# Kernel tuning notes

Measured on AMD Instinct MI355X. Metric: run time of the kernel, lower is better.

## Reference

```python
import jax, jax.numpy as jnp
import numpy as np

NH = 4  # attention heads

def rmsnorm(x, w, eps=1e-5):
    return x * jax.lax.rsqrt(jnp.mean(x * x, axis=-1, keepdims=True) + eps) * w

def gin(x, src, dst, W, b):
    # GINConv(eps=0): Linear(x + sum_{j->i} x_j)
    agg = jax.ops.segment_sum(x[src], dst, num_segments=x.shape[0])
    return (x + agg) @ W + b

def attn_pool(xb, vt, qkv_w, qkv_b, ao_w, ao_b):
    # xb: [B, Nmax, H] padded nodes (zeros participate, matching the torch code
    # which passes no key_padding_mask); vt: [T, H] virtual tokens.
    B, Nmax, H = xb.shape
    T = vt.shape[0]
    hd = H // NH
    q = (vt @ qkv_w[:, :H] + qkv_b[:H]).reshape(T, NH, hd)
    k = (xb @ qkv_w[:, H:2 * H] + qkv_b[H:2 * H]).reshape(B, Nmax, NH, hd)
    v = (xb @ qkv_w[:, 2 * H:] + qkv_b[2 * H:]).reshape(B, Nmax, NH, hd)
    scores = jnp.einsum('thd,bkhd->bhtk', q, k) / jnp.sqrt(jnp.asarray(hd, xb.dtype))
    attn = jax.nn.softmax(scores, axis=-1)
    o = jnp.einsum('bhtk,bkhd->bthd', attn, v).reshape(B, T, H)
    return o @ ao_w + ao_b

def mamba(tokens, in_w, conv_w, conv_b, x_w, dt_w, dt_b, A_log, D, out_w, norm_w, normf_w):
    # HF MambaModel with num_hidden_layers=1 (slow path), inputs_embeds path.
    B, T, H = tokens.shape
    I, K = conv_w.shape
    S = A_log.shape[1]
    R = dt_w.shape[0]
    res = tokens
    h = rmsnorm(tokens, norm_w)
    proj = h @ in_w                      # [B,T,2I]
    u, gate = jnp.split(proj, 2, axis=-1)
    up = jnp.pad(u, ((0, 0), (K - 1, 0), (0, 0)))  # causal depthwise conv1d
    conv = sum(conv_w[:, k] * up[:, k:k + T, :] for k in range(K)) + conv_b
    u = jax.nn.silu(conv)                # [B,T,I]
    ssm = u @ x_w                        # [B,T,R+2S]
    dtr, Bm, Cm = jnp.split(ssm, [R, R + S], axis=-1)
    dt = jax.nn.softplus(dtr @ dt_w + dt_b)  # [B,T,I]
    A = -jnp.exp(A_log)                  # [I,S]

    def step(hstate, inp):
        dt_t, B_t, C_t, u_t = inp        # [B,I],[B,S],[B,S],[B,I]
        dA = jnp.exp(dt_t[:, :, None] * A)
        dBu = dt_t[:, :, None] * B_t[:, None, :] * u_t[:, :, None]
        hstate = dA * hstate + dBu
        y = jnp.sum(hstate * C_t[:, None, :], axis=-1)
        return hstate, y

    h0 = jnp.zeros((B, I, S), tokens.dtype)
    xs = (dt.transpose(1, 0, 2), Bm.transpose(1, 0, 2), Cm.transpose(1, 0, 2), u.transpose(1, 0, 2))
    _, ys = jax.lax.scan(step, h0, xs)
    y = ys.transpose(1, 0, 2) + u * D
    y = y * jax.nn.silu(gate)
    out = y @ out_w                      # [B,T,H]
    return rmsnorm(res + out, normf_w)

def _forward(x, edge_index, batch, num_graphs, nodes_per_graph,
             w_in, b_in, gin_w, gin_b, vt, qkv_w, qkv_b, ao_w, ao_b,
             m_in_w, m_conv_w, m_conv_b, m_x_w, m_dt_w, m_dt_b,
             m_A_log, m_D, m_out_w, m_norm_w, m_normf_w, w_out, b_out):
    src, dst = edge_index[0], edge_index[1]
    N = x.shape[0]
    starts = jnp.searchsorted(batch, jnp.arange(num_graphs, dtype=batch.dtype))
    pos = jnp.arange(N, dtype=batch.dtype) - starts[batch]
    x = gin(x, src, dst, w_in, b_in)
    H = x.shape[-1]
    for l in range(gin_w.shape[0]):
        g = gin(x, src, dst, gin_w[l], gin_b[l])
        xb = jnp.zeros((num_graphs, nodes_per_graph, H), x.dtype).at[batch, pos].set(x)
        tokens = attn_pool(xb, vt[l], qkv_w[l], qkv_b[l], ao_w[l], ao_b[l])
        gf = mamba(tokens, m_in_w, m_conv_w, m_conv_b, m_x_w, m_dt_w, m_dt_b,
                   m_A_log, m_D, m_out_w, m_norm_w, m_normf_w)
        x = g + gf.mean(axis=1)[batch]
    x = gin(x, src, dst, w_out, b_out)
    return jax.ops.segment_sum(x, batch, num_segments=num_graphs)

def setup_inputs() -> dict:
    key = jax.random.key(0)
    ks = jax.random.split(key, 24)
    N, E, B, NPG = 131072, 2097152, 128, 1024
    IN = H = OUT = 128
    T, L = 8, 2
    I, S, R, K = 256, 16, 8, 4  # mamba: intermediate, state, dt_rank, conv kernel
    w = lambda k, s: (jax.random.normal(k, s, jnp.float32) * 0.02)
    x = jax.random.normal(ks[0], (N, IN), jnp.float32)
    edge_index = jax.random.randint(ks[1], (2, E), 0, N, jnp.int32)
    batch = (jnp.arange(N) // NPG).astype(jnp.int32)
    return dict(
        x=x, edge_index=edge_index, batch=batch, num_graphs=B, nodes_per_graph=NPG,
        w_in=w(ks[2], (IN, H)), b_in=jnp.zeros((H,), jnp.float32),
        gin_w=w(ks[3], (L, H, H)), gin_b=jnp.zeros((L, H), jnp.float32),
        vt=jax.random.normal(ks[4], (L, T, H), jnp.float32),
        qkv_w=w(ks[5], (L, H, 3 * H)), qkv_b=jnp.zeros((L, 3 * H), jnp.float32),
        ao_w=w(ks[6], (L, H, H)), ao_b=jnp.zeros((L, H), jnp.float32),
        m_in_w=w(ks[7], (H, 2 * I)),
        m_conv_w=w(ks[8], (I, K)), m_conv_b=jnp.zeros((I,), jnp.float32),
        m_x_w=w(ks[9], (I, R + 2 * S)),
        m_dt_w=w(ks[10], (R, I)), m_dt_b=jnp.full((I,), 0.1, jnp.float32),
        m_A_log=jnp.log(jnp.tile(jnp.arange(1, S + 1, dtype=jnp.float32), (I, 1))),
        m_D=jnp.ones((I,), jnp.float32),
        m_out_w=w(ks[11], (I, H)),
        m_norm_w=jnp.ones((H,), jnp.float32), m_normf_w=jnp.ones((H,), jnp.float32),
        w_out=w(ks[12], (H, OUT)), b_out=jnp.zeros((OUT,), jnp.float32),
    )

def reference(x, edge_index, batch, num_graphs, nodes_per_graph,
              w_in, b_in, gin_w, gin_b, vt, qkv_w, qkv_b, ao_w, ao_b,
              m_in_w, m_conv_w, m_conv_b, m_x_w, m_dt_w, m_dt_b,
              m_A_log, m_D, m_out_w, m_norm_w, m_normf_w, w_out, b_out):
    return _forward(x, edge_index, batch, num_graphs, nodes_per_graph,
                    w_in, b_in, gin_w, gin_b, vt, qkv_w, qkv_b, ao_w, ao_b,
                    m_in_w, m_conv_w, m_conv_b, m_x_w, m_dt_w, m_dt_b,
                    m_A_log, m_D, m_out_w, m_norm_w, m_normf_w, w_out, b_out)
```

## Files before the change

### kernel.cpp

```cpp
#include <hip/hip_runtime.h>

#define HDIM 128
#define TTOK 8
#define NPG 1024
#define NBUCK 512
#define BSHIFT 8
#define BCAP 5120
#define EPB 4096
#define PARTSZ 4160

typedef unsigned short ushort;
typedef unsigned int uint;
typedef __attribute__((ext_vector_type(8))) short short8;
typedef __attribute__((ext_vector_type(4))) float f32x4;

__device__ __forceinline__ ushort f2bf(float f) {
    unsigned int x = __float_as_uint(f);
    return (ushort)((x + 0x7FFFu + ((x >> 16) & 1u)) >> 16);
}
__device__ __forceinline__ float blo(uint u) { return __uint_as_float(u << 16); }
__device__ __forceinline__ float bhi(uint u) { return __uint_as_float(u & 0xFFFF0000u); }
__device__ __forceinline__ uint pk(float a, float b) {
    return (uint)f2bf(a) | ((uint)f2bf(b) << 16);
}

__global__ __launch_bounds__(256) void bin_kernel(const int* __restrict__ src,
    const int* __restrict__ dst, int mode, int* __restrict__ bcursor,
    uint* __restrict__ pairbuf, int E)
{
    __shared__ int lcnt[NBUCK];
    __shared__ int lbase[NBUCK];
    int tid = threadIdx.x;
    int e0 = blockIdx.x * EPB;
    for (int i = tid; i < NBUCK; i += 256) lcnt[i] = 0;
    __syncthreads();
    uint pkd[16];
    int bk[16], rk[16];
    #pragma unroll
    for (int i = 0; i < 16; ++i) {
        int e = e0 + i * 256 + tid;
        int s = (e < E) ? src[e] : 0;
        int d = (e < E) ? dst[e] : 0;
        int key = mode ? s : d;
        uint pay = mode ? (uint)(d >> 10) : (uint)s;
        if (e >= E) key = -1;
        int b = key >> BSHIFT;
        bk[i] = b;
        pkd[i] = ((uint)(key & 255) << 17) | pay;
        rk[i] = (key >= 0) ? atomicAdd(&lcnt[b], 1) : 0;
    }
    __syncthreads();
    for (int i = tid; i < NBUCK; i += 256) {
        int c = lcnt[i];
        lbase[i] = c ? atomicAdd(&bcursor[i], c) : 0;
    }
    __syncthreads();
    #pragma unroll
    for (int i = 0; i < 16; ++i) {
        if (bk[i] >= 0) {
            int slot = lbase[bk[i]] + rk[i];
            if (slot < BCAP) pairbuf[(size_t)bk[i] * BCAP + slot] = pkd[i];
        }
    }
}

__global__ __launch_bounds__(256) void bucket_sort_kernel(const uint* __restrict__ pairbuf,
    const int* __restrict__ bcount,
    int* __restrict__ ssrc, int* __restrict__ starts, int* __restrict__ countn, int N)
{
    __shared__ int sc[NBUCK];
    __shared__ int lcount[256];
    __shared__ int lcur[256];
    __shared__ int lss[BCAP];
    int b = blockIdx.x;
    int tid = threadIdx.x;
    sc[tid] = min(bcount[tid], BCAP);
    sc[tid + 256] = min(bcount[tid + 256], BCAP);
    lcount[tid] = 0;
    __syncthreads();
    for (int off = 1; off < NBUCK; off <<= 1) {
        int a0 = (tid >= off) ? sc[tid - off] : 0;
        int a1 = (tid + 256 >= off) ? sc[tid + 256 - off] : 0;
        __syncthreads();
        sc[tid] += a0; sc[tid + 256] += a1;
        __syncthreads();
    }
    int nb = min(bcount[b], BCAP);
    int base = sc[b] - nb;
    const uint* pp = pairbuf + (size_t)b * BCAP;
    for (int i = tid; i < nb; i += 256)
        atomicAdd(&lcount[(pp[i] >> 17) & 255], 1);
    __syncthreads();
    int v = lcount[tid];
    lcur[tid] = v;
    __syncthreads();
    for (int off = 1; off < 256; off <<= 1) {
        int t = (tid >= off) ? lcur[tid - off] : 0;
        __syncthreads();
        lcur[tid] += t;
        __syncthreads();
    }
    int excl = lcur[tid] - v;
    int node = b * 256 + tid;
    starts[node] = base + excl;
    countn[node] = v;
    __syncthreads();
    lcur[tid] = excl;
    __syncthreads();
    for (int i = tid; i < nb; i += 256) {
        uint p = pp[i];
        int pos = atomicAdd(&lcur[(p >> 17) & 255], 1);
        lss[pos] = (int)(p & 0x1FFFFu);
    }
    __syncthreads();
    for (int i = tid; i < nb; i += 256) ssrc[base + i] = lss[i];
    if (b == NBUCK - 1 && tid == 0) starts[N] = base + nb;
}

__global__ __launch_bounds__(256) void convert_kernel(const float* __restrict__ in,
                                                      ushort* __restrict__ outb, int n4)
{
    int i = blockIdx.x * 256 + threadIdx.x;
    if (i >= n4) return;
    float4 v = ((const float4*)in)[i];
    uint2 o;
    o.x = pk(v.x, v.y); o.y = pk(v.z, v.w);
    ((uint2*)outb)[i] = o;
}

__device__ __forceinline__ void gather16_body(const ushort* __restrict__ XS,
    const int* __restrict__ ssrc, const int* __restrict__ starts,
    const int* __restrict__ count, ushort* __restrict__ AGG, int nbase, int tid)
{
    int g = tid >> 4, lane = tid & 15;
    int node = nbase + g;
    uint4 sv = *((const uint4*)(XS + (size_t)node * HDIM) + lane);
    float a0 = blo(sv.x), a1 = bhi(sv.x), a2 = blo(sv.y), a3 = bhi(sv.y);
    float a4 = blo(sv.z), a5 = bhi(sv.z), a6 = blo(sv.w), a7 = bhi(sv.w);
    int s0 = starts[node], cn = count[node];
    for (int j0 = 0; j0 < cn; j0 += 16) {
        int myid = (j0 + lane < cn) ? ssrc[s0 + j0 + lane] : 0;
        int m = min(16, cn - j0);
        int j = 0;
        for (; j + 7 < m; j += 8) {
            uint4 u[8];
            #pragma unroll
            for (int q = 0; q < 8; ++q) {
                int sidx = __shfl(myid, j + q, 16);
                u[q] = *((const uint4*)(XS + (size_t)sidx * HDIM) + lane);
            }
            #pragma unroll
            for (int q = 0; q < 8; ++q) {
                a0 += blo(u[q].x); a1 += bhi(u[q].x);
                a2 += blo(u[q].y); a3 += bhi(u[q].y);
                a4 += blo(u[q].z); a5 += bhi(u[q].z);
                a6 += blo(u[q].w); a7 += bhi(u[q].w);
            }
        }
        for (; j + 3 < m; j += 4) {
            uint4 u[4];
            #pragma unroll
            for (int q = 0; q < 4; ++q) {
                int sidx = __shfl(myid, j + q, 16);
                u[q] = *((const uint4*)(XS + (size_t)sidx * HDIM) + lane);
            }
            #pragma unroll
            for (int q = 0; q < 4; ++q) {
                a0 += blo(u[q].x); a1 += bhi(u[q].x);
                a2 += blo(u[q].y); a3 += bhi(u[q].y);
                a4 += blo(u[q].z); a5 += bhi(u[q].z);
                a6 += blo(u[q].w); a7 += bhi(u[q].w);
            }
        }
        for (; j < m; ++j) {
            int sidx = __shfl(myid, j, 16);
            uint4 ua = *((const uint4*)(XS + (size_t)sidx * HDIM) + lane);
            a0 += blo(ua.x); a1 += bhi(ua.x);
            a2 += blo(ua.y); a3 += bhi(ua.y);
            a4 += blo(ua.z); a5 += bhi(ua.z);
            a6 += blo(ua.w); a7 += bhi(ua.w);
        }
    }
    uint4 o;
    o.x = pk(a0, a1); o.y = pk(a2, a3); o.z = pk(a4, a5); o.w = pk(a6, a7);
    *((uint4*)(AGG + (size_t)node * HDIM) + lane) = o;
}

__global__ __launch_bounds__(256) void gather_kernel(const ushort* __restrict__ XS,
    const int* __restrict__ ssrc, const int* __restrict__ starts,
    const int* __restrict__ count, ushort* __restrict__ AGG)
{
    gather16_body(XS, ssrc, starts, count, AGG, blockIdx.x * 16, threadIdx.x);
}

__device__ __forceinline__ void attn_body(const ushort* __restrict__ X,
    const float* __restrict__ P, float* __restrict__ PART, int bp, int tid)
{
    __shared__ ushort Xl[64 * 128];
    __shared__ float  St[32 * 68];
    __shared__ ushort Pl[32 * 128];
    __shared__ float lm[32], ll[32], lalpha[32];
    int b = bp >> 2, part = bp & 3;
    int wave = tid >> 6, lane = tid & 63;
    int m16 = lane & 15, quad = lane >> 4;

    for (int i = tid; i < 2048; i += 256) {
        float2 v = *(const float2*)(P + (size_t)i * 2);
        ((uint*)Pl)[i] = pk(v.x, v.y);
    }
    if (tid < 32) { lm[tid] = -1e30f; ll[tid] = 0.f; }
    __syncthreads();
    short8 aP[2][4];
    #pragma unroll
    for (int mt = 0; mt < 2; ++mt)
        #pragma unroll
        for (int kc = 0; kc < 4; ++kc)
            aP[mt][kc] = *(const short8*)&Pl[(mt * 16 + m16) * 128 + (kc * 4 + quad) * 8];
    __syncthreads();

    f32x4 oacc[2][2] = {};
    const uint4* xsg = (const uint4*)(X + (size_t)b * NPG * HDIM);

    for (int tt = 0; tt < 4; ++tt) {
        {
            const uint4* xs = xsg + (part * 4 + tt) * 1024;
            uint4* xl = (uint4*)Xl;
            for (int i = tid; i < 1024; i += 256) {
                int row = i >> 4, cc = i & 15;
                xl[row * 16 + (cc ^ (row & 15))] = xs[i];
            }
        }
        __syncthreads();
        {
            f32x4 sacc[2] = {};
            #pragma unroll
            for (int kc = 0; kc < 4; ++kc) {
                int node = wave * 16 + m16;
                short8 bx = *(const short8*)&Xl[node * 128 + (((kc * 4 + quad) ^ m16) << 3)];
                sacc[0] = __builtin_amdgcn_mfma_f32_16x16x32_bf16(aP[0][kc], bx, sacc[0], 0, 0, 0);
                sacc[1] = __builtin_amdgcn_mfma_f32_16x16x32_bf16(aP[1][kc], bx, sacc[1], 0, 0, 0);
            }
            #pragma unroll
            for (int mt = 0; mt < 2; ++mt)
                #pragma unroll
                for (int r = 0; r < 4; ++r)
                    St[(mt * 16 + quad * 4 + r) * 68 + wave * 16 + m16] = sacc[mt][r];
        }
        __syncthreads();
        {
            int j = tid >> 3, g = tid & 7;
            const float* rowp = &St[j * 68 + g * 8];
            float4 v0 = *(const float4*)(rowp);
            float4 v1 = *(const float4*)(rowp + 4);
            float mx = fmaxf(fmaxf(fmaxf(v0.x, v0.y), fmaxf(v0.z, v0.w)),
                             fmaxf(fmaxf(v1.x, v1.y), fmaxf(v1.z, v1.w)));
            mx = fmaxf(mx, __shfl_down(mx, 4, 8));
            mx = fmaxf(mx, __shfl_down(mx, 2, 8));
            mx = fmaxf(mx, __shfl_down(mx, 1, 8));
            mx = __shfl(mx, 0, 8);
            float mold = lm[j];
            float Mn = fmaxf(mold, mx);
            float alpha = __expf(mold - Mn);
            float p0 = __expf(v0.x - Mn), p1 = __expf(v0.y - Mn);
            float p2 = __expf(v0.z - Mn), p3 = __expf(v0.w - Mn);
            float p4 = __expf(v1.x - Mn), p5 = __expf(v1.y - Mn);
            float p6 = __expf(v1.z - Mn), p7 = __expf(v1.w - Mn);
            float s = ((p0 + p1) + (p2 + p3)) + ((p4 + p5) + (p6 + p7));
            s += __shfl_down(s, 4, 8);
            s += __shfl_down(s, 2, 8);
            s += __shfl_down(s, 1, 8);
            if (g == 0) {
                ll[j] = ll[j] * alpha + s;
                lm[j] = Mn;
                lalpha[j] = alpha;
            }
            uint4 u0;
            u0.x = pk(p0, p1); u0.y = pk(p2, p3); u0.z = pk(p4, p5); u0.w = pk(p6, p7);
            ((uint4*)Pl)[j * 8 + (g ^ (j & 7))] = u0;
        }
        __syncthreads();
        {
            #pragma unroll
            for (int mt = 0; mt < 2; ++mt)
                #pragma unroll
                for (int r = 0; r < 4; ++r) {
                    float a = lalpha[mt * 16 + quad * 4 + r];
                    oacc[mt][0][r] *= a;
                    oacc[mt][1][r] *= a;
                }
            #pragma unroll
            for (int kc = 0; kc < 2; ++kc) {
                short8 ap2[2], bx[2];
                #pragma unroll
                for (int mt = 0; mt < 2; ++mt)
                    ap2[mt] = *(const short8*)&Pl[(mt * 16 + m16) * 64
                                                  + (((kc * 4 + quad) ^ (m16 & 7)) << 3)];
                #pragma unroll
                for (int ntl = 0; ntl < 2; ++ntl) {
                    int cf = (2 * wave + ntl) * 16 + m16;
                    int chi = cf >> 3, clo = cf & 7;
                    short8 v;
                    #pragma unroll
                    for (int jj = 0; jj < 8; ++jj) {
                        int row = kc * 32 + quad * 8 + jj;
                        v[jj] = (short)Xl[(row << 7) + ((chi ^ (row & 15)) << 3) + clo];
                    }
                    bx[ntl] = v;
                }
                #pragma unroll
                for (int mt = 0; mt < 2; ++mt)
                    #pragma unroll
                    for (int ntl = 0; ntl < 2; ++ntl)
                        oacc[mt][ntl] = __builtin_amdgcn_mfma_f32_16x16x32_bf16(
                            ap2[mt], bx[ntl], oacc[mt][ntl], 0, 0, 0);
            }
        }
        __syncthreads();
    }
    float* PB = PART + ((size_t)b * 4 + part) * PARTSZ;
    #pragma unroll
    for (int mt = 0; mt < 2; ++mt)
        #pragma unroll
        for (int r = 0; r < 4; ++r) {
            int j = mt * 16 + quad * 4 + r;
            PB[j * 128 + (2 * wave + 0) * 16 + m16] = oacc[mt][0][r];
            PB[j * 128 + (2 * wave + 1) * 16 + m16] = oacc[mt][1][r];
        }
    if (tid < 32) { PB[4096 + tid] = lm[tid]; PB[4128 + tid] = ll[tid]; }
}
// ... 43 lines not shown
    __syncthreads();
    int wave = tid >> 6;
    int lane = tid & 63;
    int m16 = lane & 15, quad = lane >> 4;
    const short8* Xf = (const short8*)Xl;
    const short8* Wf = (const short8*)Wl;
    short8 afr[2][4];
    #pragma unroll
    for (int rt = 0; rt < 2; ++rt)
        #pragma unroll
        for (int kc = 0; kc < 4; ++kc)
            afr[rt][kc] = Xf[(wave * 32 + rt * 16 + m16) * 16 + ((kc * 4 + quad) ^ m16)];
    int graph = (int)(r0 >> 10);
    #pragma unroll
    for (int ct = 0; ct < 8; ++ct) {
        int col = ct * 16 + m16;
        short8 bfr[4];
        #pragma unroll
        for (int kc = 0; kc < 4; ++kc)
            bfr[kc] = Wf[col * 16 + ((kc * 4 + quad) ^ m16)];
        f32x4 acc0 = {0.f, 0.f, 0.f, 0.f};
        f32x4 acc1 = {0.f, 0.f, 0.f, 0.f};
        #pragma unroll
        for (int kc = 0; kc < 4; ++kc) {
            acc0 = __builtin_amdgcn_mfma_f32_16x16x32_bf16(afr[0][kc], bfr[kc], acc0, 0, 0, 0);
            acc1 = __builtin_amdgcn_mfma_f32_16x16x32_bf16(afr[1][kc], bfr[kc], acc1, 0, 0, 0);
        }
        float add = bias[col] + (GF ? GF[(size_t)graph * HDIM + col] : 0.f);
        #pragma unroll
        for (int r = 0; r < 4; ++r) {
            XD[(r0 + wave * 32 + quad * 4 + r) * HDIM + col] = f2bf(acc0[r] + add);
            XD[(r0 + wave * 32 + 16 + quad * 4 + r) * HDIM + col] = f2bf(acc1[r] + add);
        }
    }
}

__global__ __launch_bounds__(256) void attn_prep_kernel(const float* __restrict__ vt,
    const float* __restrict__ qkv_w, const float* __restrict__ qkv_b, float* __restrict__ P)
{
    __shared__ float vtl[TTOK][HDIM];
    __shared__ float q[TTOK][HDIM];
    int l = blockIdx.x;
    const float* vtp = vt + (size_t)l * TTOK * HDIM;
    const float* qw = qkv_w + (size_t)l * 128 * 384;
    const float* qb = qkv_b + (size_t)l * 384;
    float* Pp = P + (size_t)l * 4 * TTOK * HDIM;
    int tid = threadIdx.x;
    for (int i = tid; i < TTOK * HDIM; i += 256) vtl[i >> 7][i & 127] = vtp[i];
    __syncthreads();
    for (int i = tid; i < TTOK * HDIM; i += 256) {
        int t = i >> 7, j = i & 127;
        float acc = qb[j];
        for (int c = 0; c < 128; ++c) acc += vtl[t][c] * qw[c * 384 + j];
        q[t][j] = acc;
    }
    __syncthreads();
    const float scale = 0.17677669529663687f;
    for (int i = tid; i < 4 * TTOK * HDIM; i += 256) {
        int h = i >> 10, t = (i >> 7) & 7, cc = i & 127;
        float acc = 0.f;
        for (int d = 0; d < 32; ++d)
            acc += qw[cc * 384 + 128 + h * 32 + d] * q[t][h * 32 + d];
        Pp[i] = acc * scale;
    }
}

__global__ __launch_bounds__(1024) void mamba_kernel(const float* __restrict__ PART,
    const float* __restrict__ qkv_w, const float* __restrict__ qkv_b,
    const float* __restrict__ ao_w, const float* __restrict__ ao_b,
    const float* __restrict__ in_w, const float* __restrict__ conv_w,
    const float* __restrict__ conv_b, const float* __restrict__ x_w,
    const float* __restrict__ dt_w, const float* __restrict__ dt_b,
    const float* __restrict__ A_log, const float* __restrict__ Dp,
    const float* __restrict__ out_w, const float* __restrict__ norm_w,
    const float* __restrict__ normf_w, float* __restrict__ GF)
{
    constexpr int I = 256, S = 16;
    __shared__ float R[32 * 132];
    __shared__ float wgt[4][32];
    __shared__ float inv[32];
    __shared__ float tok[TTOK][HDIM];
    __shared__ float hn[TTOK][HDIM];
    __shared__ float uu[TTOK][I];
    __shared__ float gg[TTOK][I];
    __shared__ float ssm[TTOK][40];
    __shared__ float yy[TTOK][I];
    int b = blockIdx.x, tid = threadIdx.x;

    const float* PB = PART + (size_t)b * 4 * PARTSZ;
    if (tid < 32) {
        int j = tid;
        float m0 = PB[4096 + j], m1 = PB[PARTSZ + 4096 + j];
        float m2 = PB[2 * PARTSZ + 4096 + j], m3 = PB[3 * PARTSZ + 4096 + j];
        float M = fmaxf(fmaxf(m0, m1), fmaxf(m2, m3));
        float w0 = __expf(m0 - M), w1 = __expf(m1 - M);
        float w2 = __expf(m2 - M), w3 = __expf(m3 - M);
        float L = w0 * PB[4128 + j] + w1 * PB[PARTSZ + 4128 + j]
                + w2 * PB[2 * PARTSZ + 4128 + j] + w3 * PB[3 * PARTSZ + 4128 + j];
        wgt[0][j] = w0; wgt[1][j] = w1; wgt[2][j] = w2; wgt[3][j] = w3;
        inv[j] = 1.f / L;
    }
    __syncthreads();
    #pragma unroll
    for (int it = 0; it < 4; ++it) {
        int idx = it * 1024 + tid;
        int j = idx >> 7, c = idx & 127;
        float v = wgt[0][j] * PB[idx] + wgt[1][j] * PB[PARTSZ + idx]
                + wgt[2][j] * PB[2 * PARTSZ + idx] + wgt[3][j] * PB[3 * PARTSZ + idx];
        R[j * 132 + c] = v * inv[j];
    }
    __syncthreads();
    {
        int t = tid >> 7, col = tid & 127;
        int h = col >> 5;
        const float* rp = &R[(h * 8 + t) * 132];
        const float* wp = qkv_w + 256 + col;
        float acc = qkv_b[256 + col];
        for (int c = 0; c < 128; c += 8) {
            float w[8];
            #pragma unroll
            for (int q = 0; q < 8; ++q) w[q] = wp[(size_t)(c + q) * 384];
            #pragma unroll
            for (int q = 0; q < 8; ++q) acc += rp[c + q] * w[q];
        }
        hn[t][col] = acc;
    }
    __syncthreads();
    {
        int t = tid >> 7, col = tid & 127;
        const float* hp = hn[t];
        const float* wp = ao_w + col;
        float acc = ao_b[col];
        for (int k = 0; k < 128; k += 8) {
            float w[8];
            #pragma unroll
            for (int q = 0; q < 8; ++q) w[q] = wp[(size_t)(k + q) * 128];
            #pragma unroll
            for (int q = 0; q < 8; ++q) acc += hp[k + q] * w[q];
        }
        tok[t][col] = acc;
    }
    __syncthreads();

    if (tid < 512) {
        int t = tid >> 6, lane = tid & 63;
        float v0 = tok[t][lane], v1 = tok[t][lane + 64];
        float s = v0 * v0 + v1 * v1;
        #pragma unroll
        for (int off = 32; off; off >>= 1) s += __shfl_down(s, off);
        s = __shfl(s, 0);
        float r = rsqrtf(s * (1.f / 128.f) + 1e-5f);
        hn[t][lane] = v0 * r * norm_w[lane];
        hn[t][lane + 64] = v1 * r * norm_w[lane + 64];
    }
    __syncthreads();
    {
        int j = tid & 511, tq = tid >> 9;
        float acc[4] = {0.f, 0.f, 0.f, 0.f};
        const float* wp = in_w + j;
        for (int c = 0; c < 128; c += 8) {
            float w[8];
            #pragma unroll
            for (int q = 0; q < 8; ++q) w[q] = wp[(size_t)(c + q) * 512];
            #pragma unroll
            for (int q = 0; q < 8; ++q) {
                float wq = w[q];
                #pragma unroll
                for (int k = 0; k < 4; ++k) acc[k] += hn[tq * 4 + k][c + q] * wq;
            }
        }
        if (j < 256) {
            #pragma unroll
            for (int k = 0; k < 4; ++k) uu[tq * 4 + k][j] = acc[k];
        } else {
            #pragma unroll
            for (int k = 0; k < 4; ++k) gg[tq * 4 + k][j - 256] = acc[k];
        }
    }
    __syncthreads();
    if (tid < 256) {
        int i = tid;
        float cw0 = conv_w[i * 4 + 0], cw1 = conv_w[i * 4 + 1];
        float cw2 = conv_w[i * 4 + 2], cw3 = conv_w[i * 4 + 3];
        float cb = conv_b[i];
        float uv[TTOK];
        #pragma unroll
        for (int t = 0; t < TTOK; ++t) uv[t] = uu[t][i];
        #pragma unroll
        for (int t = 0; t < TTOK; ++t) {
            float a = cw3 * uv[t] + cb;
            if (t >= 1) a += cw2 * uv[t - 1];
            if (t >= 2) a += cw1 * uv[t - 2];
            if (t >= 3) a += cw0 * uv[t - 3];
            float sg = 1.f / (1.f + __expf(-a));
            uu[t][i] = a * sg;
        }
    }
    __syncthreads();
    {
        int t = tid >> 7, j = tid & 127;
        if (j < 40) {
            float acc = 0.f;
            const float* wp = x_w + j;
            const float* up = uu[t];
            for (int c = 0; c < 256; c += 8) {
                float w[8];
                #pragma unroll
                for (int q = 0; q < 8; ++q) w[q] = wp[(size_t)(c + q) * 40];
                #pragma unroll
                for (int q = 0; q < 8; ++q) acc += up[c + q] * w[q];
            }
            ssm[t][j] = acc;
        }
    }
    __syncthreads();
    if (tid < 256) {
        int i = tid;
        float dw[8];
        #pragma unroll
        for (int r = 0; r < 8; ++r) dw[r] = dt_w[r * 256 + i];
        float dtbias = dt_b[i];
        float a[S], st[S];
        #pragma unroll
        for (int s = 0; s < S; ++s) { a[s] = -__expf(A_log[i * S + s]); st[s] = 0.f; }
        float Di = Dp[i];
        for (int t = 0; t < TTOK; ++t) {
            float d = dtbias;
            #pragma unroll
            for (int r = 0; r < 8; ++r) d += ssm[t][r] * dw[r];
            d = (d > 20.f) ? d : log1pf(__expf(d));
            float ut = uu[t][i];
            float du = d * ut;
            float y = 0.f;
            #pragma unroll
            for (int s = 0; s < S; ++s) {
                float dA = __expf(d * a[s]);
                st[s] = dA * st[s] + du * ssm[t][8 + s];
                y += st[s] * ssm[t][24 + s];
            }
            y += ut * Di;
            float g = gg[t][i];
            float sg = 1.f / (1.f + __expf(-g));
            yy[t][i] = y * g * sg;
        }
    }
    __syncthreads();
    {
        int t = tid >> 7, c = tid & 127;
        float acc = tok[t][c];
        const float* wp = out_w + c;
        const float* yp = yy[t];
        for (int i = 0; i < 256; i += 8) {
            float w[8];
            #pragma unroll
            for (int q = 0; q < 8; ++q) w[q] = wp[(size_t)(i + q) * 128];
            #pragma unroll
            for (int q = 0; q < 8; ++q) acc += yp[i + q] * w[q];
        }
        hn[t][c] = acc;
    }
    __syncthreads();
    if (tid < 512) {
        int t = tid >> 6, lane = tid & 63;
        float v0 = hn[t][lane], v1 = hn[t][lane + 64];
        float s = v0 * v0 + v1 * v1;
        #pragma unroll
        for (int off = 32; off; off >>= 1) s += __shfl_down(s, off);
        s = __shfl(s, 0);
        float r = rsqrtf(s * (1.f / 128.f) + 1e-5f);
        hn[t][lane] = v0 * r * normf_w[lane];
        hn[t][lane + 64] = v1 * r * normf_w[lane + 64];
    }
    __syncthreads();
    if (tid < 128) {
        float s = 0.f;
        #pragma unroll
        for (int t = 0; t < TTOK; ++t) s += hn[t][tid];
        GF[(size_t)b * HDIM + tid] = s * (1.f / TTOK);
    }
}

__global__ __launch_bounds__(512) void final_count_kernel(const ushort* __restrict__ X,
    const uint* __restrict__ pairbuf, const int* __restrict__ bcount,
    float* __restrict__ PS2)
{
    __shared__ uint hist[128 * 66];
    __shared__ ushort Xb[128 * 128];
    int bkt = blockIdx.x, tid = threadIdx.x;
    for (int i = tid; i < 128 * 66; i += 512) hist[i] = 0u;
    __syncthreads();
// ... 92 lines not shown
    const int*   dst   = src + E;
    const float* w_in  = (const float*)d_in[5];
    const float* b_in  = (const float*)d_in[6];
    const float* gin_w = (const float*)d_in[7];
    const float* gin_b = (const float*)d_in[8];
    const float* vt    = (const float*)d_in[9];
    const float* qkv_w = (const float*)d_in[10];
    const float* qkv_b = (const float*)d_in[11];
    const float* ao_w  = (const float*)d_in[12];
    const float* ao_b  = (const float*)d_in[13];
    const float* m_in_w   = (const float*)d_in[14];
    const float* m_conv_w = (const float*)d_in[15];
    const float* m_conv_b = (const float*)d_in[16];
    const float* m_x_w    = (const float*)d_in[17];
    const float* m_dt_w   = (const float*)d_in[18];
    const float* m_dt_b   = (const float*)d_in[19];
    const float* m_A_log  = (const float*)d_in[20];
    const float* m_D      = (const float*)d_in[21];
    const float* m_out_w  = (const float*)d_in[22];
    const float* m_norm_w = (const float*)d_in[23];
    const float* m_normf_w= (const float*)d_in[24];
    const float* w_out = (const float*)d_in[25];
    const float* b_out = (const float*)d_in[26];
    float* out = (float*)d_out;

    float* GF  = (float*)d_ws;
    float* P   = GF + (size_t)B * HDIM;
    float* PART= P + 2 * 4 * TTOK * HDIM;
    int* bcursor  = (int*)(PART + (size_t)B * 4 * PARTSZ);
    int* bcursor2 = bcursor + NBUCK;
    int* count    = bcursor2 + NBUCK;
    int* starts   = count + N;
    int* ssrc     = starts + N + 8;
    uint* pairbuf = (uint*)(ssrc + E);
    float* PS2    = (float*)(pairbuf + (size_t)NBUCK * BCAP);
    ushort* AGG = (ushort*)PS2;
    ushort* XB0 = (ushort*)(PS2 + (size_t)NBUCK * 128 * 128);
    ushort* XB1 = XB0 + (size_t)N * HDIM;

    hipMemsetAsync(bcursor, 0, 2 * NBUCK * sizeof(int), stream);
    bin_kernel<<<(E + EPB - 1) / EPB, 256, 0, stream>>>(src, dst, 0, bcursor, pairbuf, E);
    bucket_sort_kernel<<<NBUCK, 256, 0, stream>>>(pairbuf, bcursor, ssrc, starts, count, N);
    bin_kernel<<<(E + EPB - 1) / EPB, 256, 0, stream>>>(src, dst, 1, bcursor2, pairbuf, E);

    attn_prep_kernel<<<2, 256, 0, stream>>>(vt, qkv_w, qkv_b, P);

    convert_kernel<<<(N * 32 + 255) / 256, 256, 0, stream>>>(x_in, XB0, N * 32);
    gather_kernel<<<N / 16, 256, 0, stream>>>(XB0, ssrc, starts, count, AGG);
    lin128_mfma_kernel<<<N / 128, 256, 0, stream>>>(AGG, w_in, b_in, nullptr, XB1);

    ushort* Xcur = XB1;
    ushort* Xnext = XB0;
    const int nAG = B * 4 + N / 16;
    for (int l = 0; l < 2; ++l) {
        attn_gather_kernel<<<nAG, 256, 0, stream>>>(Xcur, P + (size_t)l * 4 * TTOK * HDIM,
                                                    PART, ssrc, starts, count, AGG);
        mamba_kernel<<<B, 1024, 0, stream>>>(PART,
                                             qkv_w + (size_t)l * 128 * 384,
                                             qkv_b + (size_t)l * 384,
                                             ao_w + (size_t)l * 128 * 128,
                                             ao_b + (size_t)l * 128,
                                             m_in_w, m_conv_w, m_conv_b, m_x_w,
                                             m_dt_w, m_dt_b, m_A_log, m_D, m_out_w,
                                             m_norm_w, m_normf_w, GF);
        lin128_mfma_kernel<<<N / 128, 256, 0, stream>>>(AGG, gin_w + (size_t)l * 128 * 128,
                                                        gin_b + (size_t)l * 128, GF, Xnext);
        ushort* t = Xcur; Xcur = Xnext; Xnext = t;
    }

    final_count_kernel<<<NBUCK, 512, 0, stream>>>(Xcur, pairbuf, bcursor2, PS2);
    final_mm_kernel<<<B, 128, 0, stream>>>(PS2, w_out, b_out, out);

    (void)n_in; (void)out_size; (void)ws_size;
}
```

Before: 880.5 us.

## Fuse setup kernels and pre-transpose mamba weights into workspace

Merges the first edge-binning pass with the fp32-to-bf16 input conversion, and merges the attention-prep kernel with the second binning pass and a new weight-transpose stage. That stage writes transposed copies of the value, output-projection and mamba weights into workspace, so the mamba kernel reads each thread's weight row with float4 loads instead of strided scalar loads. The attention body also reuses the score buffer as its probability buffer, adding a barrier to cut LDS use. The aim is fewer launches and cheaper weight reads, but per-thread row reads are no longer coalesced across lanes, and the convert split assumes exactly NBUCK binning blocks.

```diff
diff --git a/kernel.cpp b/kernel.cpp
--- a/kernel.cpp
+++ b/kernel.cpp
@@ -9,6 +9,14 @@
 #define EPB 4096
 #define PARTSZ 4160
 
+#define MW_WVT 0
+#define MW_AOT 32768
+#define MW_INT 65536
+#define MW_XT  131072
+#define MW_DTT 141312
+#define MW_OUT 143360
+#define MW_TOT 176128
+
 typedef unsigned short ushort;
 typedef unsigned int uint;
 typedef __attribute__((ext_vector_type(8))) short short8;
@@ -24,14 +32,11 @@
     return (uint)f2bf(a) | ((uint)f2bf(b) << 16);
 }
 
-__global__ __launch_bounds__(256) void bin_kernel(const int* __restrict__ src,
+__device__ __forceinline__ void bin_body(const int* __restrict__ src,
     const int* __restrict__ dst, int mode, int* __restrict__ bcursor,
-    uint* __restrict__ pairbuf, int E)
-{
-    __shared__ int lcnt[NBUCK];
-    __shared__ int lbase[NBUCK];
-    int tid = threadIdx.x;
-    int e0 = blockIdx.x * EPB;
+    uint* __restrict__ pairbuf, int E, int e0, int tid,
+    int* lcnt, int* lbase)
+{
     for (int i = tid; i < NBUCK; i += 256) lcnt[i] = 0;
     __syncthreads();
     uint pkd[16];
@@ -64,6 +69,26 @@
     }
 }
 
+__global__ __launch_bounds__(256) void bin_conv_kernel(const int* __restrict__ src,
+    const int* __restrict__ dst, int* __restrict__ bcursor, uint* __restrict__ pairbuf,
+    int E, const float* __restrict__ xin, ushort* __restrict__ outb, int n4)
+{
+    __shared__ int lcnt[NBUCK];
+    __shared__ int lbase[NBUCK];
+    int tid = threadIdx.x;
+    int b = blockIdx.x;
+    if (b < NBUCK) {
+        bin_body(src, dst, 0, bcursor, pairbuf, E, b * EPB, tid, lcnt, lbase);
+    } else {
+        for (int i = (b - NBUCK) * 256 + tid; i < n4; i += 2048 * 256) {
+            float4 v = ((const float4*)xin)[i];
+            uint2 o;
+            o.x = pk(v.x, v.y); o.y = pk(v.z, v.w);
+            ((uint2*)outb)[i] = o;
+        }
+    }
+}
+
 __global__ __launch_bounds__(256) void bucket_sort_kernel(const uint* __restrict__ pairbuf,
     const int* __restrict__ bcount,
     int* __restrict__ ssrc, int* __restrict__ starts, int* __restrict__ countn, int N)
@@ -117,15 +142,68 @@
     if (b == NBUCK - 1 && tid == 0) starts[N] = base + nb;
 }
 
-__global__ __launch_bounds__(256) void convert_kernel(const float* __restrict__ in,
-                                                      ushort* __restrict__ outb, int n4)
-{
-    int i = blockIdx.x * 256 + threadIdx.x;
-    if (i >= n4) return;
-    float4 v = ((const float4*)in)[i];
-    uint2 o;
-    o.x = pk(v.x, v.y); o.y = pk(v.z, v.w);
-    ((uint2*)outb)[i] = o;
+__global__ __launch_bounds__(256) void prep_binsrc_kernel(const float* __restrict__ vt,
+    const float* __restrict__ qkv_w, const float* __restrict__ qkv_b, float* __restrict__ P,
+    const float* __restrict__ ao_w, const float* __restrict__ in_w,
+    const float* __restrict__ x_w, const float* __restrict__ dt_w,
+    const float* __restrict__ out_w, float* __restrict__ MW,
+    const int* __restrict__ src, const int* __restrict__ dst,
+    int* __restrict__ bcursor2, uint* __restrict__ pairbuf, int E)
+{
+    __shared__ float vtl[TTOK][HDIM];
+    __shared__ float q[TTOK][HDIM];
+    __shared__ int lcnt[NBUCK];
+    __shared__ int lbase[NBUCK];
+    int b = blockIdx.x, tid = threadIdx.x;
+    if (b < 2) {
+        int l = b;
+        const float* vtp = vt + (size_t)l * TTOK * HDIM;
+        const float* qw = qkv_w + (size_t)l * 128 * 384;
+        const float* qb = qkv_b + (size_t)l * 384;
+        float* Pp = P + (size_t)l * 4 * TTOK * HDIM;
+        for (int i = tid; i < TTOK * HDIM; i += 256) vtl[i >> 7][i & 127] = vtp[i];
+        __syncthreads();
+        for (int i = tid; i < TTOK * HDIM; i += 256) {
+            int t = i >> 7, j = i & 127;
+            float acc = qb[j];
+            for (int c = 0; c < 128; ++c) acc += vtl[t][c] * qw[c * 384 + j];
+            q[t][j] = acc;
+        }
+        __syncthreads();
+        const float scale = 0.17677669529663687f;
+        for (int i = tid; i < 4 * TTOK * HDIM; i += 256) {
+            int h = i >> 10, t = (i >> 7) & 7, cc = i & 127;
+            float acc = 0.f;
+            for (int d = 0; d < 32; ++d)
+                acc += qw[cc * 384 + 128 + h * 32 + d] * q[t][h * 32 + d];
+            Pp[i] = acc * scale;
+        }
+    } else if (b < 690) {
+        int idx = (b - 2) * 256 + tid;
+        float v;
+        if (idx < 32768) {
+            int l = idx >> 14, o = idx & 16383, col = o >> 7, c = o & 127;
+            v = qkv_w[(size_t)l * 49152 + c * 384 + 256 + col];
+        } else if (idx < 65536) {
+            int t = idx - 32768; int l = t >> 14, o = t & 16383, col = o >> 7, k = o & 127;
+            v = ao_w[(size_t)l * 16384 + k * 128 + col];
+        } else if (idx < 131072) {
+            int t = idx - 65536; int j = t >> 7, c = t & 127;
+            v = in_w[c * 512 + j];
+        } else if (idx < 141312) {
+            int t = idx - 131072; int j = t >> 8, c = t & 255;
+            v = x_w[c * 40 + j];
+        } else if (idx < 143360) {
+            int t = idx - 141312; int i = t >> 3, r = t & 7;
+            v = dt_w[r * 256 + i];
+        } else {
+            int t = idx - 143360; int c = t >> 8, i = t & 255;
+            v = out_w[i * 128 + c];
+        }
+        MW[idx] = v;
+    } else {
+        bin_body(src, dst, 1, bcursor2, pairbuf, E, (b - 690) * EPB, tid, lcnt, lbase);
+    }
 }
 
 __device__ __forceinline__ void gather16_body(const ushort* __restrict__ XS,
@@ -197,16 +275,16 @@
     const float* __restrict__ P, float* __restrict__ PART, int bp, int tid)
 {
     __shared__ ushort Xl[64 * 128];
-    __shared__ float  St[32 * 68];
-    __shared__ ushort Pl[32 * 128];
+    __shared__ float  StU[32 * 68];
     __shared__ float lm[32], ll[32], lalpha[32];
+    ushort* PlU = (ushort*)StU;
     int b = bp >> 2, part = bp & 3;
     int wave = tid >> 6, lane = tid & 63;
     int m16 = lane & 15, quad = lane >> 4;
 
     for (int i = tid; i < 2048; i += 256) {
         float2 v = *(const float2*)(P + (size_t)i * 2);
-        ((uint*)Pl)[i] = pk(v.x, v.y);
+        ((uint*)PlU)[i] = pk(v.x, v.y);
     }
     if (tid < 32) { lm[tid] = -1e30f; ll[tid] = 0.f; }
     __syncthreads();
@@ -215,7 +293,7 @@
     for (int mt = 0; mt < 2; ++mt)
         #pragma unroll
         for (int kc = 0; kc < 4; ++kc)
-            aP[mt][kc] = *(const short8*)&Pl[(mt * 16 + m16) * 128 + (kc * 4 + quad) * 8];
+            aP[mt][kc] = *(const short8*)&PlU[(mt * 16 + m16) * 128 + (kc * 4 + quad) * 8];
     __syncthreads();
 
     f32x4 oacc[2][2] = {};
@@ -244,12 +322,12 @@
             for (int mt = 0; mt < 2; ++mt)
                 #pragma unroll
                 for (int r = 0; r < 4; ++r)
-                    St[(mt * 16 + quad * 4 + r) * 68 + wave * 16 + m16] = sacc[mt][r];
+                    StU[(mt * 16 + quad * 4 + r) * 68 + wave * 16 + m16] = sacc[mt][r];
         }
         __syncthreads();
         {
             int j = tid >> 3, g = tid & 7;
-            const float* rowp = &St[j * 68 + g * 8];
+            const float* rowp = &StU[j * 68 + g * 8];
             float4 v0 = *(const float4*)(rowp);
             float4 v1 = *(const float4*)(rowp + 4);
             float mx = fmaxf(fmaxf(fmaxf(v0.x, v0.y), fmaxf(v0.z, v0.w)),
@@ -274,9 +352,10 @@
                 lm[j] = Mn;
                 lalpha[j] = alpha;
             }
+            __syncthreads();
             uint4 u0;
             u0.x = pk(p0, p1); u0.y = pk(p2, p3); u0.z = pk(p4, p5); u0.w = pk(p6, p7);
-            ((uint4*)Pl)[j * 8 + (g ^ (j & 7))] = u0;
+            ((uint4*)PlU)[j * 8 + (g ^ (j & 7))] = u0;
         }
         __syncthreads();
         {
@@ -293,8 +372,8 @@
                 short8 ap2[2], bx[2];
                 #pragma unroll
                 for (int mt = 0; mt < 2; ++mt)
-                    ap2[mt] = *(const short8*)&Pl[(mt * 16 + m16) * 64
-                                                  + (((kc * 4 + quad) ^ (m16 & 7)) << 3)];
+                    ap2[mt] = *(const short8*)&PlU[(mt * 16 + m16) * 64
+                                                   + (((kc * 4 + quad) ^ (m16 & 7)) << 3)];
                 #pragma unroll
                 for (int ntl = 0; ntl < 2; ++ntl) {
                     int cf = (2 * wave + ntl) * 16 + m16;
@@ -407,44 +486,12 @@
     }
 }
 
-__global__ __launch_bounds__(256) void attn_prep_kernel(const float* __restrict__ vt,
-    const float* __restrict__ qkv_w, const float* __restrict__ qkv_b, float* __restrict__ P)
-{
-    __shared__ float vtl[TTOK][HDIM];
-    __shared__ float q[TTOK][HDIM];
-    int l = blockIdx.x;
-    const float* vtp = vt + (size_t)l * TTOK * HDIM;
-    const float* qw = qkv_w + (size_t)l * 128 * 384;
-    const float* qb = qkv_b + (size_t)l * 384;
-    float* Pp = P + (size_t)l * 4 * TTOK * HDIM;
-    int tid = threadIdx.x;
-    for (int i = tid; i < TTOK * HDIM; i += 256) vtl[i >> 7][i & 127] = vtp[i];
-    __syncthreads();
-    for (int i = tid; i < TTOK * HDIM; i += 256) {
-        int t = i >> 7, j = i & 127;
-        float acc = qb[j];
-        for (int c = 0; c < 128; ++c) acc += vtl[t][c] * qw[c * 384 + j];
-        q[t][j] = acc;
-    }
-    __syncthreads();
-    const float scale = 0.17677669529663687f;
-    for (int i = tid; i < 4 * TTOK * HDIM; i += 256) {
-        int h = i >> 10, t = (i >> 7) & 7, cc = i & 127;
-        float acc = 0.f;
-        for (int d = 0; d < 32; ++d)
-            acc += qw[cc * 384 + 128 + h * 32 + d] * q[t][h * 32 + d];
-        Pp[i] = acc * scale;
-    }
-}
-
 __global__ __launch_bounds__(1024) void mamba_kernel(const float* __restrict__ PART,
-    const float* __restrict__ qkv_w, const float* __restrict__ qkv_b,
-    const float* __restrict__ ao_w, const float* __restrict__ ao_b,
-    const float* __restrict__ in_w, const float* __restrict__ conv_w,
-    const float* __restrict__ conv_b, const float* __restrict__ x_w,
-    const float* __restrict__ dt_w, const float* __restrict__ dt_b,
-    const float* __restrict__ A_log, const float* __restrict__ Dp,
-    const float* __restrict__ out_w, const float* __restrict__ norm_w,
+    const float* __restrict__ qkv_b, const float* __restrict__ ao_b,
+    const float* __restrict__ MW, int l,
+    const float* __restrict__ conv_w, const float* __restrict__ conv_b,
+    const float* __restrict__ dt_b, const float* __restrict__ A_log,
+    const float* __restrict__ Dp, const float* __restrict__ norm_w,
     const float* __restrict__ normf_w, float* __restrict__ GF)
 {
     constexpr int I = 256, S = 16;
@@ -486,14 +533,13 @@
         int t = tid >> 7, col = tid & 127;
         int h = col >> 5;
         const float* rp = &R[(h * 8 + t) * 132];
-        const float* wp = qkv_w + 256 + col;
+        const float* wp = MW + MW_WVT + (size_t)l * 16384 + col * 128;
         float acc = qkv_b[256 + col];
         for (int c = 0; c < 128; c += 8) {
-            float w[8];
-            #pragma unroll
-            for (int q = 0; q < 8; ++q) w[q] = wp[(size_t)(c + q) * 384];
-            #pragma unroll
-            for (int q = 0; q < 8; ++q) acc += rp[c + q] * w[q];
+            float4 wa = *(const float4*)(wp + c);
+            float4 wb = *(const float4*)(wp + c + 4);
+            acc += rp[c] * wa.x + rp[c + 1] * wa.y + rp[c + 2] * wa.z + rp[c + 3] * wa.w;
+            acc += rp[c + 4] * wb.x + rp[c + 5] * wb.y + rp[c + 6] * wb.z + rp[c + 7] * wb.w;
         }
         hn[t][col] = acc;
     }
@@ -501,14 +547,13 @@
     {
         int t = tid >> 7, col = tid & 127;
         const float* hp = hn[t];
-        const float* wp = ao_w + col;
+        const float* wp = MW + MW_AOT + (size_t)l * 16384 + col * 128;
         float acc = ao_b[col];
         for (int k = 0; k < 128; k += 8) {
-            float w[8];
-            #pragma unroll
-            for (int q = 0; q < 8; ++q) w[q] = wp[(size_t)(k + q) * 128];
-            #pragma unroll
-            for (int q = 0; q < 8; ++q) acc += hp[k + q] * w[q];
+            float4 wa = *(const float4*)(wp + k);
+            float4 wb = *(const float4*)(wp + k + 4);
+            acc += hp[k] * wa.x + hp[k + 1] * wa.y + hp[k + 2] * wa.z + hp[k + 3] * wa.w;
+            acc += hp[k + 4] * wb.x + hp[k + 5] * wb.y + hp[k + 6] * wb.z + hp[k + 7] * wb.w;
         }
         tok[t][col] = acc;
     }
@@ -529,11 +574,11 @@
     {
         int j = tid & 511, tq = tid >> 9;
         float acc[4] = {0.f, 0.f, 0.f, 0.f};
-        const float* wp = in_w + j;
+        const float* wp = MW + MW_INT + (size_t)j * 128;
         for (int c = 0; c < 128; c += 8) {
-            float w[8];
-            #pragma unroll
-            for (int q = 0; q < 8; ++q) w[q] = wp[(size_t)(c + q) * 512];
+            float4 wa = *(const float4*)(wp + c);
+            float4 wb = *(const float4*)(wp + c + 4);
+            float w[8] = {wa.x, wa.y, wa.z, wa.w, wb.x, wb.y, wb.z, wb.w};
             #pragma unroll
             for (int q = 0; q < 8; ++q) {
                 float wq = w[q];
@@ -573,14 +618,13 @@
         int t = tid >> 7, j = tid & 127;
         if (j < 40) {
             float acc = 0.f;
-            const float* wp = x_w + j;
+            const float* wp = MW + MW_XT + (size_t)j * 256;
             const float* up = uu[t];
             for (int c = 0; c < 256; c += 8) {
-                float w[8];
-                #pragma unroll
-                for (int q = 0; q < 8; ++q) w[q] = wp[(size_t)(c + q) * 40];
-                #pragma unroll
-                for (int q = 0; q < 8; ++q) acc += up[c + q] * w[q];
+                float4 wa = *(const float4*)(wp + c);
+                float4 wb = *(const float4*)(wp + c + 4);
+                acc += up[c] * wa.x + up[c + 1] * wa.y + up[c + 2] * wa.z + up[c + 3] * wa.w;
+                acc += up[c + 4] * wb.x + up[c + 5] * wb.y + up[c + 6] * wb.z + up[c + 7] * wb.w;
             }
             ssm[t][j] = acc;
         }
@@ -588,9 +632,9 @@
     __syncthreads();
     if (tid < 256) {
         int i = tid;
-        float dw[8];
-        #pragma unroll
-        for (int r = 0; r < 8; ++r) dw[r] = dt_w[r * 256 + i];
+        const float4* dp = (const float4*)(MW + MW_DTT + (size_t)i * 8);
+        float4 d0 = dp[0], d1 = dp[1];
+        float dw[8] = {d0.x, d0.y, d0.z, d0.w, d1.x, d1.y, d1.z, d1.w};
         float dtbias = dt_b[i];
         float a[S], st[S];
         #pragma unroll
@@ -620,14 +664,13 @@
     {
         int t = tid >> 7, c = tid & 127;
         float acc = tok[t][c];
-        const float* wp = out_w + c;
+        const float* wp = MW + MW_OUT + (size_t)c * 256;
         const float* yp = yy[t];
         for (int i = 0; i < 256; i += 8) {
-            float w[8];
-            #pragma unroll
-            for (int q = 0; q < 8; ++q) w[q] = wp[(size_t)(i + q) * 128];
-            #pragma unroll
-            for (int q = 0; q < 8; ++q) acc += yp[i + q] * w[q];
+            float4 wa = *(const float4*)(wp + i);
+            float4 wb = *(const float4*)(wp + i + 4);
+            acc += yp[i] * wa.x + yp[i + 1] * wa.y + yp[i + 2] * wa.z + yp[i + 3] * wa.w;
+            acc += yp[i + 4] * wb.x + yp[i + 5] * wb.y + yp[i + 6] * wb.z + yp[i + 7] * wb.w;
         }
         hn[t][c] = acc;
     }
@@ -786,20 +829,23 @@
     int* count    = bcursor2 + NBUCK;
     int* starts   = count + N;
     int* ssrc     = starts + N + 8;
-    uint* pairbuf = (uint*)(ssrc + E);
+    float* MW     = (float*)(ssrc + E);
+    uint* pairbuf = (uint*)(MW + MW_TOT);
     float* PS2    = (float*)(pairbuf + (size_t)NBUCK * BCAP);
     ushort* AGG = (ushort*)PS2;
     ushort* XB0 = (ushort*)(PS2 + (size_t)NBUCK * 128 * 128);
     ushort* XB1 = XB0 + (size_t)N * HDIM;
 
+    const int NBB = (E + EPB - 1) / EPB;
+
     hipMemsetAsync(bcursor, 0, 2 * NBUCK * sizeof(int), stream);
-    bin_kernel<<<(E + EPB - 1) / EPB, 256, 0, stream>>>(src, dst, 0, bcursor, pairbuf, E);
+    bin_conv_kernel<<<NBB + 2048, 256, 0, stream>>>(src, dst, bcursor, pairbuf, E,
+                                                    x_in, XB0, N * 32);
     bucket_sort_kernel<<<NBUCK, 256, 0, stream>>>(pairbuf, bcursor, ssrc, starts, count, N);
-    bin_kernel<<<(E + EPB - 1) / EPB, 256, 0, stream>>>(src, dst, 1, bcursor2, pairbuf, E);
-
-    attn_prep_kernel<<<2, 256, 0, stream>>>(vt, qkv_w, qkv_b, P);
-
-    convert_kernel<<<(N * 32 + 255) / 256, 256, 0, stream>>>(x_in, XB0, N * 32);
+    prep_binsrc_kernel<<<690 + NBB, 256, 0, stream>>>(vt, qkv_w, qkv_b, P,
+                                                      ao_w, m_in_w, m_x_w, m_dt_w, m_out_w, MW,
+                                                      src, dst, bcursor2, pairbuf, E);
+
     gather_kernel<<<N / 16, 256, 0, stream>>>(XB0, ssrc, starts, count, AGG);
     lin128_mfma_kernel<<<N / 128, 256, 0, stream>>>(AGG, w_in, b_in, nullptr, XB1);
 
@@ -810,12 +856,10 @@
         attn_gather_kernel<<<nAG, 256, 0, stream>>>(Xcur, P + (size_t)l * 4 * TTOK * HDIM,
                                                     PART, ssrc, starts, count, AGG);
         mamba_kernel<<<B, 1024, 0, stream>>>(PART,
-                                             qkv_w + (size_t)l * 128 * 384,
                                              qkv_b + (size_t)l * 384,
-                                             ao_w + (size_t)l * 128 * 128,
                                              ao_b + (size_t)l * 128,
-                                             m_in_w, m_conv_w, m_conv_b, m_x_w,
-                                             m_dt_w, m_dt_b, m_A_log, m_D, m_out_w,
+                                             MW, l,
+                                             m_conv_w, m_conv_b, m_dt_b, m_A_log, m_D,
                                              m_norm_w, m_normf_w, GF);
         lin128_mfma_kernel<<<N / 128, 256, 0, stream>>>(AGG, gin_w + (size_t)l * 128 * 128,
                                                         gin_b + (size_t)l * 128, GF, Xnext);
```

After: 962.1 us. 9.3% more time.

## Fuse preprocessing kernels into combined launches and alias attention shared buffers

Applied to the files above, without the earlier changes.

Edge binning and the fp32-to-bf16 input conversion now run as different block ranges of one launch. The first-layer gather, the attention-prep projection and the second binning pass are likewise merged into one kernel, dispatched by block index. The goal is to remove several small kernel launches and the serialization between independent work. Separately, the attention body keeps its probability tile in the same shared buffer as the score tile, with an extra barrier added, to cut LDS use. Block-index split points are hardcoded (NBUCK, 8194), which assumes specific E and N values.

```diff
diff --git a/kernel.cpp b/kernel.cpp
--- a/kernel.cpp
+++ b/kernel.cpp
@@ -24,14 +24,11 @@
     return (uint)f2bf(a) | ((uint)f2bf(b) << 16);
 }
 
-__global__ __launch_bounds__(256) void bin_kernel(const int* __restrict__ src,
+__device__ __forceinline__ void bin_body(const int* __restrict__ src,
     const int* __restrict__ dst, int mode, int* __restrict__ bcursor,
-    uint* __restrict__ pairbuf, int E)
-{
-    __shared__ int lcnt[NBUCK];
-    __shared__ int lbase[NBUCK];
-    int tid = threadIdx.x;
-    int e0 = blockIdx.x * EPB;
+    uint* __restrict__ pairbuf, int E, int e0, int tid,
+    int* lcnt, int* lbase)
+{
     for (int i = tid; i < NBUCK; i += 256) lcnt[i] = 0;
     __syncthreads();
     uint pkd[16];
@@ -64,6 +61,26 @@
     }
 }
 
+__global__ __launch_bounds__(256) void bin_conv_kernel(const int* __restrict__ src,
+    const int* __restrict__ dst, int* __restrict__ bcursor, uint* __restrict__ pairbuf,
+    int E, const float* __restrict__ xin, ushort* __restrict__ outb, int n4)
+{
+    __shared__ int lcnt[NBUCK];
+    __shared__ int lbase[NBUCK];
+    int tid = threadIdx.x;
+    int b = blockIdx.x;
+    if (b < NBUCK) {
+        bin_body(src, dst, 0, bcursor, pairbuf, E, b * EPB, tid, lcnt, lbase);
+    } else {
+        for (int i = (b - NBUCK) * 256 + tid; i < n4; i += 2048 * 256) {
+            float4 v = ((const float4*)xin)[i];
+            uint2 o;
+            o.x = pk(v.x, v.y); o.y = pk(v.z, v.w);
+            ((uint2*)outb)[i] = o;
+        }
+    }
+}
+
 __global__ __launch_bounds__(256) void bucket_sort_kernel(const uint* __restrict__ pairbuf,
     const int* __restrict__ bcount,
     int* __restrict__ ssrc, int* __restrict__ starts, int* __restrict__ countn, int N)
@@ -115,17 +132,6 @@
     __syncthreads();
     for (int i = tid; i < nb; i += 256) ssrc[base + i] = lss[i];
     if (b == NBUCK - 1 && tid == 0) starts[N] = base + nb;
-}
-
-__global__ __launch_bounds__(256) void convert_kernel(const float* __restrict__ in,
-                                                      ushort* __restrict__ outb, int n4)
-{
-    int i = blockIdx.x * 256 + threadIdx.x;
-    if (i >= n4) return;
-    float4 v = ((const float4*)in)[i];
-    uint2 o;
-    o.x = pk(v.x, v.y); o.y = pk(v.z, v.w);
-    ((uint2*)outb)[i] = o;
 }
 
 __device__ __forceinline__ void gather16_body(const ushort* __restrict__ XS,
@@ -186,27 +192,63 @@
     *((uint4*)(AGG + (size_t)node * HDIM) + lane) = o;
 }
 
-__global__ __launch_bounds__(256) void gather_kernel(const ushort* __restrict__ XS,
+__global__ __launch_bounds__(256) void gather_prep_kernel(const ushort* __restrict__ XS,
     const int* __restrict__ ssrc, const int* __restrict__ starts,
-    const int* __restrict__ count, ushort* __restrict__ AGG)
-{
-    gather16_body(XS, ssrc, starts, count, AGG, blockIdx.x * 16, threadIdx.x);
+    const int* __restrict__ count, ushort* __restrict__ AGG,
+    const float* __restrict__ vt, const float* __restrict__ qkv_w,
+    const float* __restrict__ qkv_b, float* __restrict__ P,
+    const int* __restrict__ src, const int* __restrict__ dst,
+    int* __restrict__ bcursor2, uint* __restrict__ pairbuf, int E)
+{
+    __shared__ float vtl[TTOK][HDIM];
+    __shared__ float q[TTOK][HDIM];
+    __shared__ int lcnt[NBUCK];
+    __shared__ int lbase[NBUCK];
+    int b = blockIdx.x, tid = threadIdx.x;
+    if (b < 2) {
+        int l = b;
+        const float* vtp = vt + (size_t)l * TTOK * HDIM;
+        const float* qw = qkv_w + (size_t)l * 128 * 384;
+        const float* qb = qkv_b + (size_t)l * 384;
+        float* Pp = P + (size_t)l * 4 * TTOK * HDIM;
+        for (int i = tid; i < TTOK * HDIM; i += 256) vtl[i >> 7][i & 127] = vtp[i];
+        __syncthreads();
+        for (int i = tid; i < TTOK * HDIM; i += 256) {
+            int t = i >> 7, j = i & 127;
+            float acc = qb[j];
+            for (int c = 0; c < 128; ++c) acc += vtl[t][c] * qw[c * 384 + j];
+            q[t][j] = acc;
+        }
+        __syncthreads();
+        const float scale = 0.17677669529663687f;
+        for (int i = tid; i < 4 * TTOK * HDIM; i += 256) {
+            int h = i >> 10, t = (i >> 7) & 7, cc = i & 127;
+            float acc = 0.f;
+            for (int d = 0; d < 32; ++d)
+                acc += qw[cc * 384 + 128 + h * 32 + d] * q[t][h * 32 + d];
+            Pp[i] = acc * scale;
+        }
+    } else if (b < 8194) {
+        gather16_body(XS, ssrc, starts, count, AGG, (b - 2) * 16, tid);
+    } else {
+        bin_body(src, dst, 1, bcursor2, pairbuf, E, (b - 8194) * EPB, tid, lcnt, lbase);
+    }
 }
 
 __device__ __forceinline__ void attn_body(const ushort* __restrict__ X,
     const float* __restrict__ P, float* __restrict__ PART, int bp, int tid)
 {
     __shared__ ushort Xl[64 * 128];
-    __shared__ float  St[32 * 68];
-    __shared__ ushort Pl[32 * 128];
+    __shared__ float  StU[32 * 68];
     __shared__ float lm[32], ll[32], lalpha[32];
+    ushort* PlU = (ushort*)StU;
     int b = bp >> 2, part = bp & 3;
     int wave = tid >> 6, lane = tid & 63;
     int m16 = lane & 15, quad = lane >> 4;
 
     for (int i = tid; i < 2048; i += 256) {
         float2 v = *(const float2*)(P + (size_t)i * 2);
-        ((uint*)Pl)[i] = pk(v.x, v.y);
+        ((uint*)PlU)[i] = pk(v.x, v.y);
     }
     if (tid < 32) { lm[tid] = -1e30f; ll[tid] = 0.f; }
     __syncthreads();
@@ -215,7 +257,7 @@
     for (int mt = 0; mt < 2; ++mt)
         #pragma unroll
         for (int kc = 0; kc < 4; ++kc)
-            aP[mt][kc] = *(const short8*)&Pl[(mt * 16 + m16) * 128 + (kc * 4 + quad) * 8];
+            aP[mt][kc] = *(const short8*)&PlU[(mt * 16 + m16) * 128 + (kc * 4 + quad) * 8];
     __syncthreads();
 
     f32x4 oacc[2][2] = {};
@@ -244,12 +286,12 @@
             for (int mt = 0; mt < 2; ++mt)
                 #pragma unroll
                 for (int r = 0; r < 4; ++r)
-                    St[(mt * 16 + quad * 4 + r) * 68 + wave * 16 + m16] = sacc[mt][r];
+                    StU[(mt * 16 + quad * 4 + r) * 68 + wave * 16 + m16] = sacc[mt][r];
         }
         __syncthreads();
         {
             int j = tid >> 3, g = tid & 7;
-            const float* rowp = &St[j * 68 + g * 8];
+            const float* rowp = &StU[j * 68 + g * 8];
             float4 v0 = *(const float4*)(rowp);
             float4 v1 = *(const float4*)(rowp + 4);
             float mx = fmaxf(fmaxf(fmaxf(v0.x, v0.y), fmaxf(v0.z, v0.w)),
@@ -274,9 +316,10 @@
                 lm[j] = Mn;
                 lalpha[j] = alpha;
             }
+            __syncthreads();
             uint4 u0;
             u0.x = pk(p0, p1); u0.y = pk(p2, p3); u0.z = pk(p4, p5); u0.w = pk(p6, p7);
-            ((uint4*)Pl)[j * 8 + (g ^ (j & 7))] = u0;
+            ((uint4*)PlU)[j * 8 + (g ^ (j & 7))] = u0;
         }
         __syncthreads();
         {
@@ -293,8 +336,8 @@
                 short8 ap2[2], bx[2];
                 #pragma unroll
                 for (int mt = 0; mt < 2; ++mt)
-                    ap2[mt] = *(const short8*)&Pl[(mt * 16 + m16) * 64
-                                                  + (((kc * 4 + quad) ^ (m16 & 7)) << 3)];
+                    ap2[mt] = *(const short8*)&PlU[(mt * 16 + m16) * 64
+                                                   + (((kc * 4 + quad) ^ (m16 & 7)) << 3)];
                 #pragma unroll
                 for (int ntl = 0; ntl < 2; ++ntl) {
                     int cf = (2 * wave + ntl) * 16 + m16;
@@ -404,36 +447,6 @@
             XD[(r0 + wave * 32 + quad * 4 + r) * HDIM + col] = f2bf(acc0[r] + add);
             XD[(r0 + wave * 32 + 16 + quad * 4 + r) * HDIM + col] = f2bf(acc1[r] + add);
         }
-    }
-}
-
-__global__ __launch_bounds__(256) void attn_prep_kernel(const float* __restrict__ vt,
-    const float* __restrict__ qkv_w, const float* __restrict__ qkv_b, float* __restrict__ P)
-{
-    __shared__ float vtl[TTOK][HDIM];
-    __shared__ float q[TTOK][HDIM];
-    int l = blockIdx.x;
-    const float* vtp = vt + (size_t)l * TTOK * HDIM;
-    const float* qw = qkv_w + (size_t)l * 128 * 384;
-    const float* qb = qkv_b + (size_t)l * 384;
-    float* Pp = P + (size_t)l * 4 * TTOK * HDIM;
-    int tid = threadIdx.x;
-    for (int i = tid; i < TTOK * HDIM; i += 256) vtl[i >> 7][i & 127] = vtp[i];
-    __syncthreads();
-    for (int i = tid; i < TTOK * HDIM; i += 256) {
-        int t = i >> 7, j = i & 127;
-        float acc = qb[j];
-        for (int c = 0; c < 128; ++c) acc += vtl[t][c] * qw[c * 384 + j];
-        q[t][j] = acc;
-    }
-    __syncthreads();
-    const float scale = 0.17677669529663687f;
-    for (int i = tid; i < 4 * TTOK * HDIM; i += 256) {
-        int h = i >> 10, t = (i >> 7) & 7, cc = i & 127;
-        float acc = 0.f;
-        for (int d = 0; d < 32; ++d)
-            acc += qw[cc * 384 + 128 + h * 32 + d] * q[t][h * 32 + d];
-        Pp[i] = acc * scale;
     }
 }
 
@@ -792,15 +805,16 @@
     ushort* XB0 = (ushort*)(PS2 + (size_t)NBUCK * 128 * 128);
     ushort* XB1 = XB0 + (size_t)N * HDIM;
 
+    const int NBB = (E + EPB - 1) / EPB;
+
     hipMemsetAsync(bcursor, 0, 2 * NBUCK * sizeof(int), stream);
-    bin_kernel<<<(E + EPB - 1) / EPB, 256, 0, stream>>>(src, dst, 0, bcursor, pairbuf, E);
+    bin_conv_kernel<<<NBB + 2048, 256, 0, stream>>>(src, dst, bcursor, pairbuf, E,
+                                                    x_in, XB0, N * 32);
     bucket_sort_kernel<<<NBUCK, 256, 0, stream>>>(pairbuf, bcursor, ssrc, starts, count, N);
-    bin_kernel<<<(E + EPB - 1) / EPB, 256, 0, stream>>>(src, dst, 1, bcursor2, pairbuf, E);
-
-    attn_prep_kernel<<<2, 256, 0, stream>>>(vt, qkv_w, qkv_b, P);
-
-    convert_kernel<<<(N * 32 + 255) / 256, 256, 0, stream>>>(x_in, XB0, N * 32);
-    gather_kernel<<<N / 16, 256, 0, stream>>>(XB0, ssrc, starts, count, AGG);
+
+    gather_prep_kernel<<<2 + N / 16 + NBB, 256, 0, stream>>>(XB0, ssrc, starts, count, AGG,
+                                                             vt, qkv_w, qkv_b, P,
+                                                             src, dst, bcursor2, pairbuf, E);
     lin128_mfma_kernel<<<N / 128, 256, 0, stream>>>(AGG, w_in, b_in, nullptr, XB1);
 
     ushort* Xcur = XB1;
```

Measured after the change: 823.3 us. 6.5% less time.
